# Kernel tuning notes

Measured on AMD Instinct MI355X. Metric: run time of the kernel, lower is better.

## Reference

```python
import jax, jax.numpy as jnp
import numpy as np

NUM_HEADS = 8

def _proj(x, W, b):
    # 1x1 conv == per-pixel linear: x [b,c,h,w], W [c_out,c_in], b [c_out]
    return jnp.einsum('bchw,oc->bohw', x, W) + b[None, :, None, None]

def setup_inputs() -> dict:
    key = jax.random.key(0)
    ks = jax.random.split(key, 5)
    b, c, h, w = 2, 256, 64, 64
    s = 0.02
    return {
        'x1': jax.random.normal(ks[0], (b, c, h, w), jnp.float32),
        'Wq': jax.random.normal(ks[1], (c, c), jnp.float32) * s,
        'bq': jnp.zeros((c,), jnp.float32),
        'Wk': jax.random.normal(ks[2], (c, c), jnp.float32) * s,
        'bk': jnp.zeros((c,), jnp.float32),
        'Wv': jax.random.normal(ks[3], (c, c), jnp.float32) * s,
        'bv': jnp.zeros((c,), jnp.float32),
        'Wo': jax.random.normal(ks[4], (c, c), jnp.float32) * s,
        'bo': jnp.zeros((c,), jnp.float32),
    }

def reference(x1, Wq, bq, Wk, bk, Wv, bv, Wo, bo):
    b, c, h, w = x1.shape
    H = NUM_HEADS
    d = c // H
    n = h * w
    scale = d ** -0.5

    def to_heads(t):
        # [b,c,h,w] -> 'b c h w -> b (h w) c' -> 'b n (H d) -> b H n d'
        # channel order: head index is the outer factor of c
        return t.reshape(b, H, d, n).transpose(0, 1, 3, 2)  # [b,H,n,d]

    q = to_heads(_proj(x1, Wq, bq))
    k = to_heads(_proj(x1, Wk, bk))
    v = to_heads(_proj(x1, Wv, bv))

    attn = jnp.einsum('bhnd,bhmd->bhnm', q, k) * scale  # [b,H,n,n]
    attn = jax.nn.softmax(attn, axis=-1)
    out = jnp.einsum('bhnm,bhmd->bhnd', attn, v)        # [b,H,n,d]
    # 'b H n d -> b n (H d)' -> 'b (h w) c -> b c h w'
    out = out.transpose(0, 2, 1, 3).reshape(b, n, c).transpose(0, 2, 1).reshape(b, c, h, w)
    return _proj(out, Wo, bo)
```

## Files before the change

kernel.cpp:

```cpp
#include <hip/hip_runtime.h>
#include <cmath>


typedef unsigned int u32;
typedef unsigned short u16;
typedef __attribute__((ext_vector_type(4))) float f32x4;
typedef __attribute__((ext_vector_type(16))) float f32x16;
typedef __attribute__((ext_vector_type(8))) short short8;
typedef __attribute__((ext_vector_type(2))) u32 u32x2;
typedef __attribute__((ext_vector_type(4))) u32 u32x4;

__device__ __forceinline__ u32 cvtpk_bf16(float a, float b) {
  u32 r; asm("v_cvt_pk_bf16_f32 %0, %1, %2" : "=v"(r) : "v"(a), "v"(b)); return r;
}
__device__ __forceinline__ void pl32swap(u32 &a, u32 &b) {
  asm("v_permlane32_swap_b32 %0, %1" : "+v"(a), "+v"(b));
}
__device__ __forceinline__ u16 f2bf(float x) { return (u16)cvtpk_bf16(x, x); }

__device__ __forceinline__ f32x16 mfma16(short8 a, short8 b, f32x16 c) {
  return __builtin_amdgcn_mfma_f32_32x32x16_bf16(a, b, c, 0, 0, 0);
}

__device__ __forceinline__ void split2(float a, float b, u32 &hw, u32 &lw) {
  u32 ua = __builtin_bit_cast(u32, a), ub = __builtin_bit_cast(u32, b);
  hw = (ua >> 16) | (ub & 0xffff0000u);
  float ra = a - __builtin_bit_cast(float, ua & 0xffff0000u);
  float rb = b - __builtin_bit_cast(float, ub & 0xffff0000u);
  lw = cvtpk_bf16(ra, rb);
}
__device__ __forceinline__ void split8(f32x4 a, f32x4 b, short8 &hf, short8 &lf) {
  u32 h0,l0,h1,l1,h2,l2,h3,l3;
  split2(a[0],a[1],h0,l0); split2(a[2],a[3],h1,l1);
  split2(b[0],b[1],h2,l2); split2(b[2],b[3],h3,l3);
  u32x4 hv = {h0,h1,h2,h3}, lv = {l0,l1,l2,l3};
  hf = __builtin_bit_cast(short8, hv);
  lf = __builtin_bit_cast(short8, lv);
}

#define LDK 40

__global__ __launch_bounds__(256) void qkv_proj_kernel(
    const float* __restrict__ X,
    const float* __restrict__ Wq, const float* __restrict__ bq,
    const float* __restrict__ Wk, const float* __restrict__ bk,
    const float* __restrict__ Wv, const float* __restrict__ bv,
    u16* __restrict__ Qh, u16* __restrict__ Kh, u16* __restrict__ V3)
{
  const int mode = blockIdx.z % 3;
  const int b    = blockIdx.z / 3;
  const float* W    = mode==0 ? Wq : (mode==1 ? Wk : Wv);
  const float* bias = mode==0 ? bq : (mode==1 ? bk : bv);
  u16* Out          = mode==0 ? Qh : (mode==1 ? Kh : V3);
  const float qmul  = mode==0 ? (0.17677669529663689f * 1.4426950408889634f) : 1.0f;

  const int c0 = blockIdx.y * 64;
  const int n0 = blockIdx.x * 128;
  const int tid = threadIdx.x;
  const int l = tid & 63, wv = tid >> 6;
  const int lane31 = l & 31, hi = l >> 5;
  const int wc = wv >> 1, wn = wv & 1;
  const int crow = c0 + wc*32 + lane31;
  const int head = blockIdx.y*2 + wc;

  __shared__ u16 xt[128 * LDK];

  f32x16 acc0 = {}, acc1 = {};

  for (int kk = 0; kk < 256; kk += 32) {
    __syncthreads();
    #pragma unroll
    for (int t = 0; t < 2; t++) {
      int task = tid + t*256;
      int pair = task >> 5;
      int nc0  = (task & 31) * 4;
      const float* px = X + ((size_t)b*256 + kk + pair*2) * 4096 + n0 + nc0;
      f32x4 xa = *(const f32x4*)px;
      f32x4 xb = *(const f32x4*)(px + 4096);
      #pragma unroll
      for (int i = 0; i < 4; i++) {
        u32 packed = cvtpk_bf16(xa[i], xb[i]);
        *(u32*)(&xt[(nc0+i)*LDK + pair*2]) = packed;
      }
    }
    __syncthreads();
    #pragma unroll
    for (int ks = 0; ks < 2; ks++) {
      const float* pw = W + (size_t)crow*256 + kk + ks*16 + hi*8;
      short8 wh, wl;
      split8(*(const f32x4*)pw, *(const f32x4*)(pw+4), wh, wl);
      short8 bf0 = *(const short8*)(&xt[(wn*64 +      lane31)*LDK + ks*16 + hi*8]);
      short8 bf1 = *(const short8*)(&xt[(wn*64 + 32 + lane31)*LDK + ks*16 + hi*8]);
      acc0 = mfma16(wh, bf0, acc0);
      acc0 = mfma16(wl, bf0, acc0);
      acc1 = mfma16(wh, bf1, acc1);
      acc1 = mfma16(wl, bf1, acc1);
    }
  }

  if (mode == 2) {
    const int kvb = (n0 + wn*64) >> 5;
    #pragma unroll
    for (int r = 0; r < 16; r++) {
      int row = (r&3) + 8*(r>>2) + 4*hi;
      float bv2 = bias[c0 + wc*32 + row];
      size_t o = (((size_t)(b*8 + head)*128 + kvb)*32 + row)*32 + lane31;
      Out[o]        = f2bf(acc0[r] + bv2);
      Out[o + 1024] = f2bf(acc1[r] + bv2);
    }
  } else {
    int n = n0 + wn*64 + lane31;
    #pragma unroll
    for (int j = 0; j < 2; j++) {
      const f32x16 &a = j ? acc1 : acc0;
      size_t base = ((size_t)(b*8 + head)*4096 + n + j*32) << 5;
      #pragma unroll
      for (int g = 0; g < 4; g++) {
        int cb = c0 + wc*32 + 8*g + 4*hi;
        int dd = 8*g + 4*hi;
        float v0 = (a[4*g+0] + bias[cb+0]) * qmul;
        float v1 = (a[4*g+1] + bias[cb+1]) * qmul;
        float v2 = (a[4*g+2] + bias[cb+2]) * qmul;
        float v3 = (a[4*g+3] + bias[cb+3]) * qmul;
        u32x2 pk = { cvtpk_bf16(v0, v1), cvtpk_bf16(v2, v3) };
        *(u32x2*)(&Out[base + dd]) = pk;
      }
    }
  }
}

__global__ __launch_bounds__(256, 4) void attn_kernel(
    const u16* __restrict__ Qh, const u16* __restrict__ Kh,
    const u16* __restrict__ V3, float* __restrict__ Os)
{
  const int fid  = blockIdx.x;
  const int xcd  = fid & 7, j = fid >> 3;
  const int bh   = xcd + 8 * (j >> 6);
  const int qgrp = j & 63;
  const int b = bh >> 3, h = bh & 7;

  const int tid = threadIdx.x, wv = tid >> 6, l = tid & 63;
  const int lane31 = l & 31, hi = l >> 5;

  const u16* qbase = Qh + (((size_t)bh*4096 + qgrp*64 + lane31) << 5) + hi*8;
  short8 qa0 = *(const short8*)(qbase);
  short8 qa1 = *(const short8*)(qbase + 16);
  short8 qb0 = *(const short8*)(qbase + 1024);
  short8 qb1 = *(const short8*)(qbase + 1040);

  f32x16 accA = {}, accB = {};
  float lsA0 = 0.f, lsA1 = 0.f, lsB0 = 0.f, lsB1 = 0.f;

  const u16* kbase = Kh + (((size_t)bh*4096 + lane31) << 5) + hi*8;
  const u16* vbase = V3 + ((size_t)bh << 17) + lane31*32 + hi*8;

  for (int kvo = 0; kvo < 1024; kvo += 32) {
    const int kv = wv*1024 + kvo;
    const u16* kp = kbase + ((size_t)kv << 5);
    const u16* vp = vbase + ((size_t)(kv >> 5) << 10);
    short8 kc0 = *(const short8*)(kp);
    short8 kc1 = *(const short8*)(kp + 16);
    short8 vc0 = *(const short8*)(vp);
    short8 vc1 = *(const short8*)(vp + 16);

    {
      f32x16 s = {};
      s = mfma16(kc0, qa0, s);
      s = mfma16(kc1, qa1, s);
      #pragma unroll
      for (int r = 0; r < 16; r++) s[r] = __builtin_amdgcn_exp2f(s[r]);
      lsA0 += (s[0]+s[1]) + (s[4]+s[5]);
      lsA1 += (s[2]+s[3]) + (s[6]+s[7]);
      lsA0 += (s[8]+s[9]) + (s[12]+s[13]);
      lsA1 += (s[10]+s[11]) + (s[14]+s[15]);
      u32 a0 = cvtpk_bf16(s[0],s[1]),   b0 = cvtpk_bf16(s[4],s[5]);
      u32 c1 = cvtpk_bf16(s[2],s[3]),   d1 = cvtpk_bf16(s[6],s[7]);
      u32 e0 = cvtpk_bf16(s[8],s[9]),   f0 = cvtpk_bf16(s[12],s[13]);
      u32 g1 = cvtpk_bf16(s[10],s[11]), h1 = cvtpk_bf16(s[14],s[15]);
      pl32swap(a0,b0); pl32swap(c1,d1); pl32swap(e0,f0); pl32swap(g1,h1);
      u32x4 u0 = {a0,c1,b0,d1}, u1 = {e0,g1,f0,h1};
      accA = mfma16(__builtin_bit_cast(short8,u0), vc0, accA);
      accA = mfma16(__builtin_bit_cast(short8,u1), vc1, accA);
    }
    {
      f32x16 s = {};
      s = mfma16(kc0, qb0, s);
      s = mfma16(kc1, qb1, s);
      #pragma unroll
      for (int r = 0; r < 16; r++) s[r] = __builtin_amdgcn_exp2f(s[r]);
      lsB0 += (s[0]+s[1]) + (s[4]+s[5]);
      lsB1 += (s[2]+s[3]) + (s[6]+s[7]);
      lsB0 += (s[8]+s[9]) + (s[12]+s[13]);
      lsB1 += (s[10]+s[11]) + (s[14]+s[15]);
      u32 a0 = cvtpk_bf16(s[0],s[1]),   b0 = cvtpk_bf16(s[4],s[5]);
      u32 c1 = cvtpk_bf16(s[2],s[3]),   d1 = cvtpk_bf16(s[6],s[7]);
      u32 e0 = cvtpk_bf16(s[8],s[9]),   f0 = cvtpk_bf16(s[12],s[13]);
      u32 g1 = cvtpk_bf16(s[10],s[11]), h1 = cvtpk_bf16(s[14],s[15]);
      pl32swap(a0,b0); pl32swap(c1,d1); pl32swap(e0,f0); pl32swap(g1,h1);
      u32x4 u0 = {a0,c1,b0,d1}, u1 = {e0,g1,f0,h1};
      accB = mfma16(__builtin_bit_cast(short8,u0), vc0, accB);
      accB = mfma16(__builtin_bit_cast(short8,u1), vc1, accB);
    }
  }

  __shared__ float accbA[4][64][17], accbB[4][64][17];
  __shared__ float lsbA[4][64], lsbB[4][64];

  lsbA[wv][l] = lsA0 + lsA1;
  lsbB[wv][l] = lsB0 + lsB1;
  #pragma unroll
  for (int r = 0; r < 16; r++) { accbA[wv][l][r] = accA[r]; accbB[wv][l][r] = accB[r]; }
  __syncthreads();

  float LtA = (lsbA[0][l]+lsbA[1][l]) + (lsbA[2][l]+lsbA[3][l]);
  float LtB = (lsbB[0][l]+lsbB[1][l]) + (lsbB[2][l]+lsbB[3][l]);
  LtA += __shfl_xor(LtA, 32);
  LtB += __shfl_xor(LtB, 32);
  float LiA = 1.0f / LtA, LiB = 1.0f / LtB;

  #pragma unroll
  for (int i = 0; i < 4; i++) {
    int r = wv*4 + i;
    float oA = (accbA[0][l][r]+accbA[1][l][r]) + (accbA[2][l][r]+accbA[3][l][r]);
    float oB = (accbB[0][l][r]+accbB[1][l][r]) + (accbB[2][l][r]+accbB[3][l][r]);
    int row = (r&3) + 8*(r>>2) + 4*hi;
    float LrA = __shfl(LiA, row);
    float LrB = __shfl(LiB, row);
    int qgA = qgrp*64 + row;
    Os[(((size_t)b*4096 + qgA) << 8) + h*32 + lane31]      = oA * LrA;
    Os[(((size_t)b*4096 + qgA + 32) << 8) + h*32 + lane31] = oB * LrB;
  }
}

__global__ __launch_bounds__(256) void oproj_kernel(
    const float* __restrict__ O, const float* __restrict__ Wo,
    const float* __restrict__ bo, float* __restrict__ Out)
{
  const int b = blockIdx.z, c0 = blockIdx.y*64, n0 = blockIdx.x*64;
  const int tid = threadIdx.x, wv = tid >> 6, l = tid & 63;
  const int lane31 = l & 31, hi = l >> 5;
  const int wc = wv >> 1, wn = wv & 1;
  const int crow = c0 + wc*32 + lane31;
  f32x16 acc = {};

  for (int kk = 0; kk < 256; kk += 16) {
    const float* pw = Wo + (size_t)crow*256 + kk + hi*8;
    short8 wh, wl;
    split8(*(const f32x4*)pw, *(const f32x4*)(pw+4), wh, wl);
    const float* po = O + (((size_t)b*4096 + n0 + wn*32 + lane31) << 8) + kk + hi*8;
    short8 oh, ol;
    split8(*(const f32x4*)po, *(const f32x4*)(po+4), oh, ol);
    acc = mfma16(wh, oh, acc);
    acc = mfma16(wh, ol, acc);
    acc = mfma16(wl, oh, acc);
  }
  #pragma unroll
  for (int r = 0; r < 16; r++) {
    int row = (r&3) + 8*(r>>2) + 4*hi;
    int c = c0 + wc*32 + row;
    float bv = bo[c];
    size_t o = ((size_t)b*256 + c)*4096 + n0 + wn*32 + lane31;
    Out[o] = acc[r] + bv;
  }
}

extern "C" void kernel_launch(void* const* d_in, const int* in_sizes, int n_in,
                              void* d_out, int out_size, void* d_ws, size_t ws_size,
                              hipStream_t stream) {
  const float* x1 = (const float*)d_in[0];
  const float* Wq = (const float*)d_in[1];
  const float* bq = (const float*)d_in[2];
  const float* Wk = (const float*)d_in[3];
  const float* bk = (const float*)d_in[4];
  const float* Wv = (const float*)d_in[5];
  const float* bv = (const float*)d_in[6];
  const float* Wo = (const float*)d_in[7];
  const float* bo = (const float*)d_in[8];

  const size_t NEL = (size_t)2 * 4096 * 256;
  u16* Qh = (u16*)d_ws;
  u16* Kh = Qh + NEL;
  u16* V3 = Kh + NEL;
  float* Os = (float*)(V3 + NEL);
  float* out = (float*)d_out;

  qkv_proj_kernel<<<dim3(32, 4, 6), 256, 0, stream>>>(x1, Wq, bq, Wk, bk, Wv, bv, Qh, Kh, V3);
  attn_kernel<<<dim3(1024), 256, 0, stream>>>(Qh, Kh, V3, Os);
  oproj_kernel<<<dim3(64, 4, 2), 256, 0, stream>>>(Os, Wo, bo, out);
}
```

Before: 159.8 us.

## Pre-pack inputs and weights into MFMA fragment layout and prefetch K/V in attention

Adds a prep kernel that transposes X to bf16 and pre-splits all weights (Q scale folded in) into hi/lo bf16 planes stored in MFMA-fragment order. The QKV, attention and output-projection kernels then read fragments with single vector loads instead of doing LDS staging and per-use splitting. The attention kernel software-prefetches the next K/V tile and writes its output already split and fragment-packed for the output projection. This removes redundant conversion work and strided loads, at the cost of an extra kernel launch and extra workspace traffic.

```diff
diff --git a/kernel.cpp b/kernel.cpp
--- a/kernel.cpp
+++ b/kernel.cpp
@@ -7,7 +7,6 @@
 typedef __attribute__((ext_vector_type(4))) float f32x4;
 typedef __attribute__((ext_vector_type(16))) float f32x16;
 typedef __attribute__((ext_vector_type(8))) short short8;
-typedef __attribute__((ext_vector_type(2))) u32 u32x2;
 typedef __attribute__((ext_vector_type(4))) u32 u32x4;
 
 __device__ __forceinline__ u32 cvtpk_bf16(float a, float b) {
@@ -38,130 +37,164 @@
   lf = __builtin_bit_cast(short8, lv);
 }
 
-#define LDK 40
-
-__global__ __launch_bounds__(256) void qkv_proj_kernel(
+__device__ __forceinline__ int rowmap(int r, int hi) {
+  return (r & 3) + 8 * ((r >> 2) & 1) + 4 * hi + 16 * (r >> 3);
+}
+
+#define QMUL (0.17677669529663689f * 1.4426950408889634f)
+#define WPLANE 65536
+#define WMAT  131072
+
+__global__ __launch_bounds__(256) void prep_kernel(
     const float* __restrict__ X,
-    const float* __restrict__ Wq, const float* __restrict__ bq,
-    const float* __restrict__ Wk, const float* __restrict__ bk,
-    const float* __restrict__ Wv, const float* __restrict__ bv,
-    u16* __restrict__ Qh, u16* __restrict__ Kh, u16* __restrict__ V3)
+    const float* __restrict__ Wq, const float* __restrict__ Wk,
+    const float* __restrict__ Wv, const float* __restrict__ Wo,
+    u16* __restrict__ Xa, u16* __restrict__ Wpk)
 {
-  const int mode = blockIdx.z % 3;
-  const int b    = blockIdx.z / 3;
-  const float* W    = mode==0 ? Wq : (mode==1 ? Wk : Wv);
-  const float* bias = mode==0 ? bq : (mode==1 ? bk : bv);
-  u16* Out          = mode==0 ? Qh : (mode==1 ? Kh : V3);
-  const float qmul  = mode==0 ? (0.17677669529663689f * 1.4426950408889634f) : 1.0f;
-
-  const int c0 = blockIdx.y * 64;
-  const int n0 = blockIdx.x * 128;
-  const int tid = threadIdx.x;
-  const int l = tid & 63, wv = tid >> 6;
-  const int lane31 = l & 31, hi = l >> 5;
-  const int wc = wv >> 1, wn = wv & 1;
-  const int crow = c0 + wc*32 + lane31;
-  const int head = blockIdx.y*2 + wc;
-
-  __shared__ u16 xt[128 * LDK];
-
-  f32x16 acc0 = {}, acc1 = {};
-
-  for (int kk = 0; kk < 256; kk += 32) {
+  const int bx = blockIdx.x, tid = threadIdx.x;
+  if (bx < 256) {
+    __shared__ float lt[32 * 257];
+    const int b = bx >> 7, ntile = bx & 127, n0 = ntile * 32;
+    const int nn = tid & 31, cg = tid >> 5;
+    #pragma unroll 4
+    for (int i = 0; i < 32; i++) {
+      int c = i * 8 + cg;
+      lt[nn * 257 + c] = X[((size_t)b * 256 + c) * 4096 + n0 + nn];
+    }
     __syncthreads();
+    const int lane = tid & 63, w = tid >> 6;
+    const int l31 = lane & 31, fh = lane >> 5;
     #pragma unroll
-    for (int t = 0; t < 2; t++) {
-      int task = tid + t*256;
-      int pair = task >> 5;
-      int nc0  = (task & 31) * 4;
-      const float* px = X + ((size_t)b*256 + kk + pair*2) * 4096 + n0 + nc0;
-      f32x4 xa = *(const f32x4*)px;
-      f32x4 xb = *(const f32x4*)(px + 4096);
-      #pragma unroll
-      for (int i = 0; i < 4; i++) {
-        u32 packed = cvtpk_bf16(xa[i], xb[i]);
-        *(u32*)(&xt[(nc0+i)*LDK + pair*2]) = packed;
+    for (int kk = 0; kk < 4; kk++) {
+      int kt = w * 4 + kk;
+      const float* p = &lt[l31 * 257 + kt * 16 + fh * 8];
+      u32x4 pk = { cvtpk_bf16(p[0],p[1]), cvtpk_bf16(p[2],p[3]),
+                   cvtpk_bf16(p[4],p[5]), cvtpk_bf16(p[6],p[7]) };
+      *(u32x4*)(&Xa[(((size_t)b * 128 + ntile) * 16 + kt) * 512 + lane * 8]) = pk;
+    }
+  } else {
+    const int j = (bx - 256) * 256 + tid;
+    const int lane = j & 63, ct = (j >> 6) & 7, kt = (j >> 9) & 15, mat = j >> 13;
+    const float* W = mat == 0 ? Wq : (mat == 1 ? Wk : (mat == 2 ? Wv : Wo));
+    const int c = ct * 32 + (lane & 31);
+    const int k0 = kt * 16 + (lane >> 5) * 8;
+    f32x4 a = *(const f32x4*)(W + (size_t)c * 256 + k0);
+    f32x4 b = *(const f32x4*)(W + (size_t)c * 256 + k0 + 4);
+    if (mat == 0) {
+      #pragma unroll
+      for (int i = 0; i < 4; i++) { a[i] *= QMUL; b[i] *= QMUL; }
+    }
+    short8 wh, wl; split8(a, b, wh, wl);
+    size_t base = ((size_t)mat * 2) * WPLANE + ((size_t)kt * 8 + ct) * 512 + lane * 8;
+    *(short8*)(&Wpk[base]) = wh;
+    *(short8*)(&Wpk[base + WPLANE]) = wl;
+  }
+}
+
+__global__ __launch_bounds__(256) void qkv_kernel(
+    const u16* __restrict__ Xa, const u16* __restrict__ Wpk,
+    const float* __restrict__ bq, const float* __restrict__ bk,
+    const float* __restrict__ bv,
+    u16* __restrict__ Qf, u16* __restrict__ Kf, u16* __restrict__ V3)
+{
+  const int z = blockIdx.z, mode = z % 3, b = z / 3;
+  const int tid = threadIdx.x, lane = tid & 63, wv = tid >> 6;
+  const int wn = wv & 1, wcH = wv >> 1;
+  const int ntile = blockIdx.x * 2 + wn;
+  const int l31 = lane & 31, fh = lane >> 5;
+
+  const u16* Amat = Xa + ((size_t)b * 128 + ntile) * 8192;
+  const u16* Bmat = Wpk + (size_t)mode * WMAT;
+
+  f32x16 acc[4] = {{}, {}, {}, {}};
+  for (int kt = 0; kt < 16; kt++) {
+    short8 xa = *(const short8*)(Amat + kt * 512 + lane * 8);
+    #pragma unroll
+    for (int i = 0; i < 4; i++) {
+      int ct = wcH * 4 + i;
+      const u16* wp = Bmat + ((size_t)kt * 8 + ct) * 512 + lane * 8;
+      short8 wh = *(const short8*)(wp);
+      short8 wl = *(const short8*)(wp + WPLANE);
+      acc[i] = mfma16(wh, xa, acc[i]);
+      acc[i] = mfma16(wl, xa, acc[i]);
+    }
+  }
+
+  const float* bias = mode == 0 ? bq : (mode == 1 ? bk : bv);
+  const float bscale = mode == 0 ? QMUL : 1.0f;
+
+  if (mode == 2) {
+    #pragma unroll
+    for (int i = 0; i < 4; i++) {
+      int head = wcH * 4 + i;
+      size_t tb = (((size_t)(b * 8 + head) * 128 + ntile) * 32) * 32;
+      #pragma unroll
+      for (int r = 0; r < 16; r++) {
+        int dv = rowmap(r, fh);
+        V3[tb + (size_t)dv * 32 + l31] = f2bf(acc[i][r] + bias[head * 32 + dv]);
       }
     }
-    __syncthreads();
+  } else {
+    u16* Out = mode == 0 ? Qf : Kf;
     #pragma unroll
-    for (int ks = 0; ks < 2; ks++) {
-      const float* pw = W + (size_t)crow*256 + kk + ks*16 + hi*8;
-      short8 wh, wl;
-      split8(*(const f32x4*)pw, *(const f32x4*)(pw+4), wh, wl);
-      short8 bf0 = *(const short8*)(&xt[(wn*64 +      lane31)*LDK + ks*16 + hi*8]);
-      short8 bf1 = *(const short8*)(&xt[(wn*64 + 32 + lane31)*LDK + ks*16 + hi*8]);
-      acc0 = mfma16(wh, bf0, acc0);
-      acc0 = mfma16(wl, bf0, acc0);
-      acc1 = mfma16(wh, bf1, acc1);
-      acc1 = mfma16(wl, bf1, acc1);
-    }
-  }
-
-  if (mode == 2) {
-    const int kvb = (n0 + wn*64) >> 5;
-    #pragma unroll
-    for (int r = 0; r < 16; r++) {
-      int row = (r&3) + 8*(r>>2) + 4*hi;
-      float bv2 = bias[c0 + wc*32 + row];
-      size_t o = (((size_t)(b*8 + head)*128 + kvb)*32 + row)*32 + lane31;
-      Out[o]        = f2bf(acc0[r] + bv2);
-      Out[o + 1024] = f2bf(acc1[r] + bv2);
-    }
-  } else {
-    int n = n0 + wn*64 + lane31;
-    #pragma unroll
-    for (int j = 0; j < 2; j++) {
-      const f32x16 &a = j ? acc1 : acc0;
-      size_t base = ((size_t)(b*8 + head)*4096 + n + j*32) << 5;
-      #pragma unroll
-      for (int g = 0; g < 4; g++) {
-        int cb = c0 + wc*32 + 8*g + 4*hi;
-        int dd = 8*g + 4*hi;
-        float v0 = (a[4*g+0] + bias[cb+0]) * qmul;
-        float v1 = (a[4*g+1] + bias[cb+1]) * qmul;
-        float v2 = (a[4*g+2] + bias[cb+2]) * qmul;
-        float v3 = (a[4*g+3] + bias[cb+3]) * qmul;
-        u32x2 pk = { cvtpk_bf16(v0, v1), cvtpk_bf16(v2, v3) };
-        *(u32x2*)(&Out[base + dd]) = pk;
+    for (int i = 0; i < 4; i++) {
+      int head = wcH * 4 + i;
+      size_t nb = (((size_t)(b * 8 + head) * 128 + ntile) * 2) * 512;
+      #pragma unroll
+      for (int kt2 = 0; kt2 < 2; kt2++) {
+        float v[8];
+        #pragma unroll
+        for (int e = 0; e < 8; e++) {
+          int c = head * 32 + rowmap(kt2 * 8 + e, fh);
+          v[e] = acc[i][kt2 * 8 + e] + bscale * bias[c];
+        }
+        u32x4 pk = { cvtpk_bf16(v[0],v[1]), cvtpk_bf16(v[2],v[3]),
+                     cvtpk_bf16(v[4],v[5]), cvtpk_bf16(v[6],v[7]) };
+        *(u32x4*)(&Out[nb + (size_t)kt2 * 512 + lane * 8]) = pk;
       }
     }
   }
 }
 
 __global__ __launch_bounds__(256, 4) void attn_kernel(
-    const u16* __restrict__ Qh, const u16* __restrict__ Kh,
-    const u16* __restrict__ V3, float* __restrict__ Os)
+    const u16* __restrict__ Qf, const u16* __restrict__ Kf,
+    const u16* __restrict__ V3, u16* __restrict__ OaH, u16* __restrict__ OaL)
 {
-  const int fid  = blockIdx.x;
-  const int xcd  = fid & 7, j = fid >> 3;
-  const int bh   = xcd + 8 * (j >> 6);
+  const int fid = blockIdx.x;
+  const int xcd = fid & 7, j = fid >> 3;
+  const int bh = xcd + 8 * (j >> 6);
   const int qgrp = j & 63;
   const int b = bh >> 3, h = bh & 7;
 
-  const int tid = threadIdx.x, wv = tid >> 6, l = tid & 63;
-  const int lane31 = l & 31, hi = l >> 5;
-
-  const u16* qbase = Qh + (((size_t)bh*4096 + qgrp*64 + lane31) << 5) + hi*8;
-  short8 qa0 = *(const short8*)(qbase);
-  short8 qa1 = *(const short8*)(qbase + 16);
-  short8 qb0 = *(const short8*)(qbase + 1024);
-  short8 qb1 = *(const short8*)(qbase + 1040);
+  const int tid = threadIdx.x, wv = tid >> 6, lane = tid & 63;
+  const int l31 = lane & 31, fh = lane >> 5;
+
+  const u16* qfb = Qf + (size_t)bh * 131072 + (size_t)(qgrp * 2) * 1024 + lane * 8;
+  short8 qa0 = *(const short8*)(qfb);
+  short8 qa1 = *(const short8*)(qfb + 512);
+  short8 qb0 = *(const short8*)(qfb + 1024);
+  short8 qb1 = *(const short8*)(qfb + 1536);
+
+  const u16* kfb = Kf + (size_t)bh * 131072;
+  const u16* vfb = V3 + (size_t)bh * 131072;
 
   f32x16 accA = {}, accB = {};
   float lsA0 = 0.f, lsA1 = 0.f, lsB0 = 0.f, lsB1 = 0.f;
 
-  const u16* kbase = Kh + (((size_t)bh*4096 + lane31) << 5) + hi*8;
-  const u16* vbase = V3 + ((size_t)bh << 17) + lane31*32 + hi*8;
-
-  for (int kvo = 0; kvo < 1024; kvo += 32) {
-    const int kv = wv*1024 + kvo;
-    const u16* kp = kbase + ((size_t)kv << 5);
-    const u16* vp = vbase + ((size_t)(kv >> 5) << 10);
-    short8 kc0 = *(const short8*)(kp);
-    short8 kc1 = *(const short8*)(kp + 16);
-    short8 vc0 = *(const short8*)(vp);
-    short8 vc1 = *(const short8*)(vp + 16);
+  int kvt = wv * 32;
+  short8 kc0 = *(const short8*)(kfb + (size_t)kvt * 1024 + lane * 8);
+  short8 kc1 = *(const short8*)(kfb + (size_t)kvt * 1024 + 512 + lane * 8);
+  short8 vc0 = *(const short8*)(vfb + (size_t)kvt * 1024 + l31 * 32 + fh * 8);
+  short8 vc1 = *(const short8*)(vfb + (size_t)kvt * 1024 + l31 * 32 + fh * 8 + 16);
+
+  for (int it = 0; it < 32; it++) {
+    int nx = wv * 32 + ((it + 1) & 31);
+    const u16* kpn = kfb + (size_t)nx * 1024 + lane * 8;
+    const u16* vpn = vfb + (size_t)nx * 1024 + l31 * 32 + fh * 8;
+    short8 kn0 = *(const short8*)(kpn);
+    short8 kn1 = *(const short8*)(kpn + 512);
+    short8 vn0 = *(const short8*)(vpn);
+    short8 vn1 = *(const short8*)(vpn + 16);
 
     {
       f32x16 s = {};
@@ -201,66 +234,72 @@
       accB = mfma16(__builtin_bit_cast(short8,u0), vc0, accB);
       accB = mfma16(__builtin_bit_cast(short8,u1), vc1, accB);
     }
+    kc0 = kn0; kc1 = kn1; vc0 = vn0; vc1 = vn1;
   }
 
   __shared__ float accbA[4][64][17], accbB[4][64][17];
-  __shared__ float lsbA[4][64], lsbB[4][64];
-
-  lsbA[wv][l] = lsA0 + lsA1;
-  lsbB[wv][l] = lsB0 + lsB1;
+  __shared__ float lsb2[2][4][64];
+
+  lsb2[0][wv][lane] = lsA0 + lsA1;
+  lsb2[1][wv][lane] = lsB0 + lsB1;
   #pragma unroll
-  for (int r = 0; r < 16; r++) { accbA[wv][l][r] = accA[r]; accbB[wv][l][r] = accB[r]; }
+  for (int r = 0; r < 16; r++) { accbA[wv][lane][r] = accA[r]; accbB[wv][lane][r] = accB[r]; }
   __syncthreads();
 
-  float LtA = (lsbA[0][l]+lsbA[1][l]) + (lsbA[2][l]+lsbA[3][l]);
-  float LtB = (lsbB[0][l]+lsbB[1][l]) + (lsbB[2][l]+lsbB[3][l]);
-  LtA += __shfl_xor(LtA, 32);
-  LtB += __shfl_xor(LtB, 32);
-  float LiA = 1.0f / LtA, LiB = 1.0f / LtB;
-
+  const int set = wv & 1, kt = wv >> 1;
+  const int qp = l31;
+  float Lt = 0.f;
   #pragma unroll
-  for (int i = 0; i < 4; i++) {
-    int r = wv*4 + i;
-    float oA = (accbA[0][l][r]+accbA[1][l][r]) + (accbA[2][l][r]+accbA[3][l][r]);
-    float oB = (accbB[0][l][r]+accbB[1][l][r]) + (accbB[2][l][r]+accbB[3][l][r]);
-    int row = (r&3) + 8*(r>>2) + 4*hi;
-    float LrA = __shfl(LiA, row);
-    float LrB = __shfl(LiB, row);
-    int qgA = qgrp*64 + row;
-    Os[(((size_t)b*4096 + qgA) << 8) + h*32 + lane31]      = oA * LrA;
-    Os[(((size_t)b*4096 + qgA + 32) << 8) + h*32 + lane31] = oB * LrB;
-  }
+  for (int w2 = 0; w2 < 4; w2++) Lt += lsb2[set][w2][qp] + lsb2[set][w2][qp + 32];
+  const float Linv = 1.0f / Lt;
+
+  const int hi_w = (qp >> 2) & 1;
+  const int rr = (qp & 3) + ((qp >> 3) << 2);
+  float o[8];
+  #pragma unroll
+  for (int e = 0; e < 8; e++) {
+    int idx = (kt * 16 + fh * 8 + e) + 32 * hi_w;
+    float v = set ? (accbB[0][idx][rr] + accbB[1][idx][rr] + accbB[2][idx][rr] + accbB[3][idx][rr])
+                  : (accbA[0][idx][rr] + accbA[1][idx][rr] + accbA[2][idx][rr] + accbA[3][idx][rr]);
+    o[e] = v * Linv;
+  }
+  f32x4 o0 = {o[0], o[1], o[2], o[3]}, o1 = {o[4], o[5], o[6], o[7]};
+  short8 oh, ol; split8(o0, o1, oh, ol);
+  const int qt = qgrp * 2 + set, ktg = h * 2 + kt;
+  size_t addr = (((size_t)b * 128 + qt) * 16 + ktg) * 512 + lane * 8;
+  *(short8*)(&OaH[addr]) = oh;
+  *(short8*)(&OaL[addr]) = ol;
 }
 
 __global__ __launch_bounds__(256) void oproj_kernel(
-    const float* __restrict__ O, const float* __restrict__ Wo,
-    const float* __restrict__ bo, float* __restrict__ Out)
+    const u16* __restrict__ OaH, const u16* __restrict__ OaL,
+    const u16* __restrict__ Wpk, const float* __restrict__ bo,
+    float* __restrict__ Out)
 {
-  const int b = blockIdx.z, c0 = blockIdx.y*64, n0 = blockIdx.x*64;
-  const int tid = threadIdx.x, wv = tid >> 6, l = tid & 63;
-  const int lane31 = l & 31, hi = l >> 5;
-  const int wc = wv >> 1, wn = wv & 1;
-  const int crow = c0 + wc*32 + lane31;
+  const int b = blockIdx.z, ct = blockIdx.y;
+  const int tid = threadIdx.x, lane = tid & 63, wv = tid >> 6;
+  const int ntile = blockIdx.x * 4 + wv;
+  const int l31 = lane & 31, fh = lane >> 5;
+
+  const u16* Wo = Wpk + (size_t)3 * WMAT;
+  const u16* Ob = OaH + ((size_t)b * 128 + ntile) * 8192;
+  const u16* Ol = OaL + ((size_t)b * 128 + ntile) * 8192;
+
   f32x16 acc = {};
-
-  for (int kk = 0; kk < 256; kk += 16) {
-    const float* pw = Wo + (size_t)crow*256 + kk + hi*8;
-    short8 wh, wl;
-    split8(*(const f32x4*)pw, *(const f32x4*)(pw+4), wh, wl);
-    const float* po = O + (((size_t)b*4096 + n0 + wn*32 + lane31) << 8) + kk + hi*8;
-    short8 oh, ol;
-    split8(*(const f32x4*)po, *(const f32x4*)(po+4), oh, ol);
+  for (int kt = 0; kt < 16; kt++) {
+    const u16* wp = Wo + ((size_t)kt * 8 + ct) * 512 + lane * 8;
+    short8 wh = *(const short8*)(wp);
+    short8 wl = *(const short8*)(wp + WPLANE);
+    short8 oh = *(const short8*)(Ob + kt * 512 + lane * 8);
+    short8 ol = *(const short8*)(Ol + kt * 512 + lane * 8);
     acc = mfma16(wh, oh, acc);
     acc = mfma16(wh, ol, acc);
     acc = mfma16(wl, oh, acc);
   }
   #pragma unroll
   for (int r = 0; r < 16; r++) {
-    int row = (r&3) + 8*(r>>2) + 4*hi;
-    int c = c0 + wc*32 + row;
-    float bv = bo[c];
-    size_t o = ((size_t)b*256 + c)*4096 + n0 + wn*32 + lane31;
-    Out[o] = acc[r] + bv;
+    int c = ct * 32 + rowmap(r, fh);
+    Out[((size_t)b * 256 + c) * 4096 + ntile * 32 + l31] = acc[r] + bo[c];
   }
 }
 
@@ -278,13 +317,17 @@
   const float* bo = (const float*)d_in[8];
 
   const size_t NEL = (size_t)2 * 4096 * 256;
-  u16* Qh = (u16*)d_ws;
-  u16* Kh = Qh + NEL;
-  u16* V3 = Kh + NEL;
-  float* Os = (float*)(V3 + NEL);
+  u16* Xa  = (u16*)d_ws;
+  u16* Qf  = Xa + NEL;
+  u16* Kf  = Qf + NEL;
+  u16* V3  = Kf + NEL;
+  u16* OaL = V3 + NEL;
+  u16* Wpk = OaL + NEL;
+  u16* OaH = Xa;
   float* out = (float*)d_out;
 
-  qkv_proj_kernel<<<dim3(32, 4, 6), 256, 0, stream>>>(x1, Wq, bq, Wk, bk, Wv, bv, Qh, Kh, V3);
-  attn_kernel<<<dim3(1024), 256, 0, stream>>>(Qh, Kh, V3, Os);
-  oproj_kernel<<<dim3(64, 4, 2), 256, 0, stream>>>(Os, Wo, bo, out);
-}
+  prep_kernel<<<dim3(384), 256, 0, stream>>>(x1, Wq, Wk, Wv, Wo, Xa, Wpk);
+  qkv_kernel<<<dim3(64, 1, 6), 256, 0, stream>>>(Xa, Wpk, bq, bk, bv, Qf, Kf, V3);
+  attn_kernel<<<dim3(1024), 256, 0, stream>>>(Qf, Kf, V3, OaH, OaL);
+  oproj_kernel<<<dim3(32, 8, 2), 256, 0, stream>>>(OaH, OaL, Wpk, bo, out);
+}
```

Result: faster. 148.1 us (-7.4%).
